# Kernel tuning notes

Measured on AMD Instinct MI355X. Metric: run time of the kernel, lower is better.

## Reference

```python
import jax, jax.numpy as jnp
import numpy as np
from jax import lax

COMMITMENT_WEIGHT = 0.25
EMA_DECAY = 0.99
EPS = 1e-5


def setup_inputs() -> dict:
    key = jax.random.key(0)
    k1, k2, k3 = jax.random.split(key, 3)
    B, L, D, K = 32, 512, 384, 8192
    z = jax.random.normal(k1, (B, L, D), dtype=jnp.float32)
    codebook = jax.random.normal(k2, (K, D), dtype=jnp.float32)
    ema_cluster_size = jnp.zeros((K,), dtype=jnp.float32)
    ema_embed_sum = jax.random.normal(k3, (K, D), dtype=jnp.float32)
    return {"z": z, "codebook": codebook, "ema_cluster_size": ema_cluster_size, "ema_embed_sum": ema_embed_sum}


def reference(z, codebook, ema_cluster_size, ema_embed_sum):
    B, L, D = z.shape
    K = codebook.shape[0]
    flat_z = z.reshape(-1, D)  # [N, D]

    # squared L2 distance to every code: [N, K]
    dist = (
        jnp.sum(flat_z * flat_z, axis=-1, keepdims=True)
        + jnp.sum(codebook * codebook, axis=-1)[None, :]
        - 2.0 * (flat_z @ codebook.T)
    )
    indices = jnp.argmin(dist, axis=-1)  # [N]
    quantized = codebook[indices].reshape(B, L, D)

    # EMA codebook update (training-mode, no-grad in original)
    cluster_size = jax.ops.segment_sum(jnp.ones_like(indices, dtype=flat_z.dtype), indices, num_segments=K)
    embed_sum = jax.ops.segment_sum(flat_z, indices, num_segments=K)  # [K, D]
    new_cluster_size = ema_cluster_size * EMA_DECAY + (1.0 - EMA_DECAY) * cluster_size
    new_embed_sum = ema_embed_sum * EMA_DECAY + (1.0 - EMA_DECAY) * embed_sum
    n = jnp.sum(new_cluster_size)
    cluster_size_smoothed = (new_cluster_size + EPS) / (n + K * EPS) * n
    new_codebook = new_embed_sum / cluster_size_smoothed[:, None]

    commitment_loss = jnp.mean((z - lax.stop_gradient(quantized)) ** 2)
    codebook_loss = jnp.mean((quantized - lax.stop_gradient(z)) ** 2)
    loss = codebook_loss + COMMITMENT_WEIGHT * commitment_loss

    # straight-through estimator
    quantized_st = z + lax.stop_gradient(quantized - z)
    return (quantized_st, indices.reshape(B, L), loss, new_cluster_size, new_embed_sum, new_codebook)
```

## Files before the change

### kernel.cpp

```cpp
#include <hip/hip_runtime.h>
#include <math.h>

#define N_TOK 16384
#define DDIM  384
#define KCODE 8192
#define EMA   0.99f
#define EPS_F 1e-5f
#define MARGIN 0.5f
#define NB 32

typedef _Float16 f16x8 __attribute__((ext_vector_type(8)));
typedef float    f32x4 __attribute__((ext_vector_type(4)));

#define OFF_PD1    0UL
#define OFF_PI1    2097152UL
#define OFF_PD2    4194304UL
#define OFF_CBH    6291456UL
#define OFF_PRD    0UL
#define OFF_PRI    1048576UL
#define OFF_TOKL   0UL
#define OFF_OFFS   65536UL
#define OFF_CURS   98560UL
#define OFF_WSIDX  12582912UL
#define OFF_COUNTS 12648448UL
#define OFF_SUMSQ  12681216UL
#define OFF_NACC   12681220UL
#define OFF_CNORM  12681472UL
#define OFF_FLIST  12714240UL
#define OFF_FCNT   12779776UL
#define OFF_PSUM   12780032UL

typedef __attribute__((address_space(1))) const unsigned int gas_uint;
typedef __attribute__((address_space(3))) unsigned int       las_uint;
__device__ __forceinline__ void gload_lds16(const void* g, void* l) {
    __builtin_amdgcn_global_load_lds((gas_uint*)g, (las_uint*)l, 16, 0, 0);
}

__global__ void cnorm_kernel(const float* __restrict__ cb, float* __restrict__ cnorm) {
    int wave = (blockIdx.x * blockDim.x + threadIdx.x) >> 6;
    int lane = threadIdx.x & 63;
    if (wave >= KCODE) return;
    const float* row = cb + (size_t)wave * DDIM;
    float s = 0.f;
    #pragma unroll
    for (int r = 0; r < 6; r++) { float v = row[lane + 64 * r]; s += v * v; }
    #pragma unroll
    for (int off = 32; off > 0; off >>= 1) s += __shfl_down(s, off, 64);
    if (lane == 0) cnorm[wave] = s;
}

__global__ void convert_kernel(const float* __restrict__ z, const float* __restrict__ cb,
                               _Float16* __restrict__ zh, _Float16* __restrict__ cbh) {
    size_t e = ((size_t)blockIdx.x * blockDim.x + threadIdx.x) * 8;
    const size_t NZ = (size_t)N_TOK * DDIM;
    const float* s;
    _Float16* d;
    if (e < NZ) { s = z + e; d = zh + e; }
    else        { s = cb + (e - NZ); d = cbh + (e - NZ); }
    float4 v0 = *(const float4*)(s);
    float4 v1 = *(const float4*)(s + 4);
    f16x8 h;
    h[0]=(_Float16)v0.x; h[1]=(_Float16)v0.y; h[2]=(_Float16)v0.z; h[3]=(_Float16)v0.w;
    h[4]=(_Float16)v1.x; h[5]=(_Float16)v1.y; h[6]=(_Float16)v1.z; h[7]=(_Float16)v1.w;
    *(f16x8*)d = h;
}

__launch_bounds__(512)
__global__ void argmin16_kernel(const _Float16* __restrict__ zh, const _Float16* __restrict__ cbh,
                                const float* __restrict__ cnorm,
                                float* __restrict__ pd1, int* __restrict__ pi1,
                                float* __restrict__ pd2) {
    __shared__ _Float16 As[128 * 32];
    __shared__ _Float16 Bs[256 * 32];
    __shared__ float xd1[128 * 4];
    __shared__ float xd2[128 * 4];
    __shared__ int   xi1[128 * 4];

    const int tid  = threadIdx.x;
    const int lane = tid & 63;
    const int wv   = tid >> 6;
    const int wy   = wv >> 2;
    const int wx   = wv & 3;
    const int m0   = blockIdx.x * 128;
    const int n0   = blockIdx.y * 256;
    const int l15  = lane & 15;
    const int l4   = lane >> 4;
    const int csw  = (l15 >> 1) & 3;

    f32x4 acc[4][4];
    #pragma unroll
    for (int i = 0; i < 4; i++)
        #pragma unroll
        for (int j = 0; j < 4; j++) acc[i][j] = (f32x4){0.f, 0.f, 0.f, 0.f};

    const int arow = tid >> 2;
    const int jch  = (tid & 3) ^ ((tid >> 3) & 3);
    const _Float16* a_src  = zh  + (size_t)(m0 + arow) * DDIM + jch * 8;
    const _Float16* b_src0 = cbh + (size_t)(n0 + arow) * DDIM + jch * 8;
    const _Float16* b_src1 = cbh + (size_t)(n0 + 128 + arow) * DDIM + jch * 8;
    _Float16* a_dst  = As + wv * 512;
    _Float16* b_dst0 = Bs + wv * 512;
    _Float16* b_dst1 = Bs + wv * 512 + 4096;

    for (int kc = 0; kc < DDIM; kc += 32) {
        gload_lds16(a_src + kc,  a_dst);
        gload_lds16(b_src0 + kc, b_dst0);
        gload_lds16(b_src1 + kc, b_dst1);
        __syncthreads();
        f16x8 af[4], bf[4];
        #pragma unroll
        for (int im = 0; im < 4; im++)
            af[im] = *(const f16x8*)(As + (wy * 64 + im * 16 + l15) * 32 + (l4 ^ csw) * 8);
        #pragma unroll
        for (int in = 0; in < 4; in++)
            bf[in] = *(const f16x8*)(Bs + (wx * 64 + in * 16 + l15) * 32 + (l4 ^ csw) * 8);
        #pragma unroll
        for (int im = 0; im < 4; im++)
            #pragma unroll
            for (int in = 0; in < 4; in++)
                acc[im][in] = __builtin_amdgcn_mfma_f32_16x16x32_f16(af[im], bf[in], acc[im][in], 0, 0, 0);
        __syncthreads();
    }

    float cn[4]; int cid[4];
    #pragma unroll
    for (int in = 0; in < 4; in++) {
        cid[in] = n0 + wx * 64 + in * 16 + l15;
        cn[in] = cnorm[cid[in]];
    }
    #pragma unroll
    for (int im = 0; im < 4; im++) {
        #pragma unroll
        for (int reg = 0; reg < 4; reg++) {
            float d1 = cn[0] - 2.f * acc[im][0][reg];
            int   i1 = cid[0];
            float d2 = 3.4e38f;
            #pragma unroll
            for (int in = 1; in < 4; in++) {
                float dd = cn[in] - 2.f * acc[im][in][reg];
                if (dd < d1) { d2 = d1; d1 = dd; i1 = cid[in]; }
                else d2 = fminf(d2, dd);
            }
            #pragma unroll
            for (int off = 1; off < 16; off <<= 1) {
                float od1 = __shfl_xor(d1, off, 16);
                int   oi1 = __shfl_xor(i1, off, 16);
                float od2 = __shfl_xor(d2, off, 16);
                if (od1 < d1 || (od1 == d1 && oi1 < i1)) { d2 = fminf(d1, od2); d1 = od1; i1 = oi1; }
                else d2 = fminf(d2, od1);
            }
            if (l15 == 0) {
                int tl = wy * 64 + im * 16 + l4 * 4 + reg;
                xd1[tl * 4 + wx] = d1; xi1[tl * 4 + wx] = i1; xd2[tl * 4 + wx] = d2;
            }
        }
    }
    __syncthreads();
    if (tid < 128) {
        float d1 = xd1[tid * 4], d2 = xd2[tid * 4];
        int   i1 = xi1[tid * 4];
        #pragma unroll
        for (int x = 1; x < 4; x++) {
            float od1 = xd1[tid * 4 + x], od2 = xd2[tid * 4 + x];
            int   oi1 = xi1[tid * 4 + x];
            if (od1 < d1 || (od1 == d1 && oi1 < i1)) { d2 = fminf(d1, od2); d1 = od1; i1 = oi1; }
            else d2 = fminf(d2, od1);
        }
        size_t o = (size_t)blockIdx.y * N_TOK + m0 + tid;
        pd1[o] = d1; pi1[o] = i1; pd2[o] = d2;
    }
}

__global__ void topmerge_kernel(const float* __restrict__ pd1, const int* __restrict__ pi1,
                                const float* __restrict__ pd2,
                                int* __restrict__ ws_idx, float* __restrict__ out_idx,
                                int* __restrict__ fcnt, int* __restrict__ flist) {
    int t = blockIdx.x * blockDim.x + threadIdx.x;
    if (t >= N_TOK) return;
    float d1 = pd1[t], d2 = pd2[t];
    int   i1 = pi1[t];
    for (int nb = 1; nb < NB; nb++) {
        size_t o = (size_t)nb * N_TOK + t;
        float od1 = pd1[o], od2 = pd2[o];
        int   oi1 = pi1[o];
        if (od1 < d1 || (od1 == d1 && oi1 < i1)) { d2 = fminf(d1, od2); d1 = od1; i1 = oi1; }
        else d2 = fminf(d2, od1);
    }
    ws_idx[t] = i1;
    out_idx[t] = (float)i1;
    if (d2 - d1 < MARGIN) {
        int s = atomicAdd(fcnt, 1);
        flist[s] = t;
    }
}

__launch_bounds__(256)
__global__ void rescore_kernel(const float* __restrict__ z, const float* __restrict__ cb,
                               const float* __restrict__ cnorm,
                               const int* __restrict__ flist, const int* __restrict__ fcnt,
                               float* __restrict__ prd, int* __restrict__ pri) {
    __shared__ float zt[8 * 384];
    __shared__ float rd[8 * 4];
    __shared__ int   ri[8 * 4];
    const int tid = threadIdx.x;
    const int lane = tid & 63, wv = tid >> 6;
    const int s = blockIdx.x;
    const int count = fcnt[0];
    for (int g = blockIdx.y; g * 8 < count; g += 256) {
        #pragma unroll
        for (int r = 0; r < 3; r++) {
            int q = tid + r * 256;
            int j = q / 96, d4 = q % 96;
            int slot = g * 8 + j; if (slot >= count) slot = count - 1;
            int tok = flist[slot];
            *(float4*)(zt + j * 384 + d4 * 4) = *(const float4*)(z + (size_t)tok * DDIM + d4 * 4);
        }
        __syncthreads();
        float bd[8]; int bi[8];
        #pragma unroll
        for (int j = 0; j < 8; j++) { bd[j] = 3.4e38f; bi[j] = 0; }
        #pragma unroll
        for (int cc = 0; cc < 2; cc++) {
            int c = s * 512 + cc * 256 + tid;
            const float* cr = cb + (size_t)c * DDIM;
            float a[8];
            #pragma unroll
            for (int j = 0; j < 8; j++) a[j] = 0.f;
            for (int d4 = 0; d4 < 96; d4++) {
                float4 cv = *(const float4*)(cr + d4 * 4);
                #pragma unroll
                for (int j = 0; j < 8; j++) {
                    float4 zv = *(const float4*)(zt + j * 384 + d4 * 4);
                    a[j] = fmaf(zv.x, cv.x, a[j]);
                    a[j] = fmaf(zv.y, cv.y, a[j]);
                    a[j] = fmaf(zv.z, cv.z, a[j]);
                    a[j] = fmaf(zv.w, cv.w, a[j]);
                }
            }
            float cnv = cnorm[c];
            #pragma unroll
            for (int j = 0; j < 8; j++) {
                float dd = cnv - 2.f * a[j];
                if (dd < bd[j]) { bd[j] = dd; bi[j] = c; }
            }
        }
        #pragma unroll
        for (int j = 0; j < 8; j++) {
            float d = bd[j]; int i = bi[j];
            #pragma unroll
            for (int off = 32; off > 0; off >>= 1) {
                float od = __shfl_xor(d, off, 64);
                int   oi = __shfl_xor(i, off, 64);
                if (od < d || (od == d && oi < i)) { d = od; i = oi; }
            }
            if (lane == 0) { rd[j * 4 + wv] = d; ri[j * 4 + wv] = i; }
        }
        __syncthreads();
        if (tid < 8) {
            float d = rd[tid * 4]; int i = ri[tid * 4];
            #pragma unroll
            for (int x = 1; x < 4; x++) {
                float od = rd[tid * 4 + x]; int oi = ri[tid * 4 + x];
                if (od < d || (od == d && oi < i)) { d = od; i = oi; }
            }
            int slot = g * 8 + tid; if (slot >= count) slot = count - 1;
            int tok = flist[slot];
            prd[(size_t)s * N_TOK + tok] = d;
            pri[(size_t)s * N_TOK + tok] = i;
        }
        __syncthreads();
    }
}

__global__ void rsmerge_kernel(const float* __restrict__ prd, const int* __restrict__ pri,
                               const int* __restrict__ flist, const int* __restrict__ fcnt,
                               int* __restrict__ ws_idx, float* __restrict__ out_idx) {
    int slot = blockIdx.x * blockDim.x + threadIdx.x;
    if (slot >= fcnt[0]) return;
    int tok = flist[slot];
    float d = prd[tok]; int i = pri[tok];
    for (int s = 1; s < 16; s++) {
        float od = prd[(size_t)s * N_TOK + tok];
        int   oi = pri[(size_t)s * N_TOK + tok];
        if (od < d || (od == d && oi < i)) { d = od; i = oi; }
    }
    ws_idx[tok] = i;
    out_idx[tok] = (float)i;
}

__global__ void quantize_kernel(const float* __restrict__ z, const float* __restrict__ cb,
                                const int* __restrict__ ws_idx,
                                float* __restrict__ out_q,
                                float* __restrict__ counts, float* __restrict__ psum) {
    __shared__ float sm[4];
    int t = (blockIdx.x * blockDim.x + threadIdx.x) >> 6;
    int lane = threadIdx.x & 63, wv = threadIdx.x >> 6;
    int k = ws_idx[t];
    const float* zr = z + (size_t)t * DDIM;
    const float* cr = cb + (size_t)k * DDIM;
    float* qr = out_q + (size_t)t * DDIM;
    float s = 0.f;
    #pragma unroll
    for (int r = 0; r < 6; r++) {
        int d = lane + 64 * r;
        float zv = zr[d];
        float qv = cr[d];
        qr[d] = qv;
        float df = zv - qv;
        s += df * df;
    }
    #pragma unroll
    for (int off = 32; off > 0; off >>= 1) s += __shfl_down(s, off, 64);
    if (lane == 0) {
        sm[wv] = s;
        atomicAdd(counts + k, 1.0f);
    }
    __syncthreads();
    if (threadIdx.x == 0) psum[blockIdx.x] = sm[0] + sm[1] + sm[2] + sm[3];
}

__global__ void scan_kernel(const float* __restrict__ counts,
                            int* __restrict__ offs, int* __restrict__ curs) {
    __shared__ int ps[1024];
    const int t = threadIdx.x;
    const int base = t * 8;
    int loc[8]; int s = 0;
    #pragma unroll
    for (int i = 0; i < 8; i++) { int c = (int)(counts[base + i] + 0.5f); loc[i] = s; s += c; }
    ps[t] = s;
    __syncthreads();
    for (int off = 1; off < 1024; off <<= 1) {
        int v = ps[t];
        int add = (t >= off) ? ps[t - off] : 0;
        __syncthreads();
        ps[t] = v + add;
        __syncthreads();
    }
    int excl = (t == 0) ? 0 : ps[t - 1];
    #pragma unroll
    for (int i = 0; i < 8; i++) {
        int o = excl + loc[i];
        offs[base + i] = o;
        curs[base + i] = o;
    }
    if (t == 1023) offs[KCODE] = ps[1023];
}

__global__ void fill_kernel(const int* __restrict__ ws_idx,
                            int* __restrict__ curs, int* __restrict__ toklist) {
    int t = blockIdx.x * blockDim.x + threadIdx.x;
    if (t >= N_TOK) return;
    int k = ws_idx[t];
    int slot = atomicAdd(curs + k, 1);
    toklist[slot] = t;
}

__global__ void cluster_kernel(const float* __restrict__ ema_cs, const float* __restrict__ counts,
                               float* __restrict__ out_ncs, float* __restrict__ n_acc,
                               const float* __restrict__ psum, float* __restrict__ out_loss) {
    int i = blockIdx.x * blockDim.x + threadIdx.x;
    float v = 0.f;
    if (i < KCODE) {
        v = EMA * ema_cs[i] + (1.f - EMA) * counts[i];
        out_ncs[i] = v;
    }
    __shared__ float sm[4];
    __shared__ float sm2[4];
    int lane = threadIdx.x & 63, w = threadIdx.x >> 6;
    #pragma unroll
    for (int off = 32; off > 0; off >>= 1) v += __shfl_down(v, off, 64);
    if (lane == 0) sm[w] = v;
    __syncthreads();
    if (threadIdx.x == 0) atomicAdd(n_acc, sm[0] + sm[1] + sm[2] + sm[3]);
    if (blockIdx.x == 0) {
        float s = 0.f;
        for (int j = threadIdx.x; j < 4096; j += 256) s += psum[j];
        #pragma unroll
        for (int off = 32; off > 0; off >>= 1) s += __shfl_down(s, off, 64);
        if (lane == 0) sm2[w] = s;
        __syncthreads();
        if (threadIdx.x == 0)
            out_loss[0] = 1.25f * (sm2[0] + sm2[1] + sm2[2] + sm2[3]) / (float)(N_TOK * DDIM);
    }
}

__global__ void codebook_fused_kernel(const float* __restrict__ z,
                                      const int* __restrict__ offs, const int* __restrict__ toklist,
                                      const float* __restrict__ ema_es,
                                      const float* __restrict__ ncs, const float* __restrict__ n_acc,
                                      float* __restrict__ out_es, float* __restrict__ out_cb) {
    int k = (blockIdx.x * blockDim.x + threadIdx.x) >> 6;
    int lane = threadIdx.x & 63;
    if (k >= KCODE) return;
    int o0 = offs[k], o1 = offs[k + 1];
    float sum[6] = {0.f, 0.f, 0.f, 0.f, 0.f, 0.f};
    for (int s = o0; s < o1; s++) {
        int tok = toklist[s];
        const float* zr = z + (size_t)tok * DDIM;
        #pragma unroll
        for (int r = 0; r < 6; r++) sum[r] += zr[lane + 64 * r];
    }
    float n = n_acc[0];
    float smooth = (ncs[k] + EPS_F) / (n + (float)KCODE * EPS_F) * n;
    float inv = 1.f / smooth;
    const float* er = ema_es + (size_t)k * DDIM;
    float* oes = out_es + (size_t)k * DDIM;
    float* ocb = out_cb + (size_t)k * DDIM;
    #pragma unroll
    for (int r = 0; r < 6; r++) {
        int d = lane + 64 * r;
        float es = EMA * er[d] + (1.f - EMA) * sum[r];
        oes[d] = es;
        ocb[d] = es * inv;
    }
}

extern "C" void kernel_launch(void* const* d_in, const int* in_sizes, int n_in,
                              void* d_out, int out_size, void* d_ws, size_t ws_size,
                              hipStream_t stream) {
    const float* z       = (const float*)d_in[0];
    const float* cb      = (const float*)d_in[1];
    const float* ema_cs  = (const float*)d_in[2];
    const float* ema_es  = (const float*)d_in[3];

    float* out      = (float*)d_out;
    float* out_q    = out;
    float* out_idx  = out + 6291456;
    float* out_loss = out + 6307840;
    float* out_ncs  = out + 6307841;
    float* out_es   = out + 6316033;
    float* out_cb   = out + 9461761;

    char* w = (char*)d_ws;
    float* pd1    = (float*)(w + OFF_PD1);
    int*   pi1    = (int*)  (w + OFF_PI1);
    float* pd2    = (float*)(w + OFF_PD2);
    _Float16* cbh = (_Float16*)(w + OFF_CBH);
    float* prd    = (float*)(w + OFF_PRD);
    int*   pri    = (int*)  (w + OFF_PRI);
    int*   toklist= (int*)  (w + OFF_TOKL);
    int*   offs   = (int*)  (w + OFF_OFFS);
    int*   curs   = (int*)  (w + OFF_CURS);
    float* cnorm  = (float*)(w + OFF_CNORM);
    int*   flist  = (int*)  (w + OFF_FLIST);
    int*   fcnt   = (int*)  (w + OFF_FCNT);
    int*   ws_idx = (int*)  (w + OFF_WSIDX);
    float* counts = (float*)(w + OFF_COUNTS);
    float* psum   = (float*)(w + OFF_PSUM);
    float* n_acc  = (float*)(w + OFF_NACC);

    _Float16* zh = (_Float16*)out;

    hipMemsetAsync(w + OFF_FCNT, 0, 256, stream);
    hipMemsetAsync(w + OFF_COUNTS, 0, 32768 + 256, stream);

    cnorm_kernel<<<KCODE * 64 / 256, 256, 0, stream>>>(cb, cnorm);

    convert_kernel<<<4608, 256, 0, stream>>>(z, cb, zh, cbh);

    dim3 grid_am(N_TOK / 128, KCODE / 256, 1);
    argmin16_kernel<<<grid_am, 512, 0, stream>>>(zh, cbh, cnorm, pd1, pi1, pd2);

    topmerge_kernel<<<N_TOK / 256, 256, 0, stream>>>(pd1, pi1, pd2, ws_idx, out_idx, fcnt, flist);

    dim3 grid_rs(16, 256, 1);
    rescore_kernel<<<grid_rs, 256, 0, stream>>>(z, cb, cnorm, flist, fcnt, prd, pri);
    rsmerge_kernel<<<N_TOK / 256, 256, 0, stream>>>(prd, pri, flist, fcnt, ws_idx, out_idx);

    quantize_kernel<<<N_TOK * 64 / 256, 256, 0, stream>>>(z, cb, ws_idx, out_q, counts, psum);
    scan_kernel<<<1, 1024, 0, stream>>>(counts, offs, curs);
    fill_kernel<<<N_TOK / 256, 256, 0, stream>>>(ws_idx, curs, toklist);
    cluster_kernel<<<(KCODE + 255) / 256, 256, 0, stream>>>(ema_cs, counts, out_ncs, n_acc, psum, out_loss);
    codebook_fused_kernel<<<KCODE * 64 / 256, 256, 0, stream>>>(z, offs, toklist, ema_es, out_ncs, n_acc, out_es, out_cb);
}
```

Before: 616.1 us.

## Rescore ambiguous tokens only against candidate blocks within margin band

Replaces the exhaustive fp32 rescore of flagged tokens over all 8192 codes, along with its separate merge kernel, with a per-wave rescore. Each wave handles one token and visits only the 256-code blocks whose fp16 best distance lies within MARGIN of the global best. Each lane walks one codebook row per iteration, so loads are uncoalesced, and correctness still depends on the fp16 error staying inside the margin band.

After: 594.8 us. -3.5%, faster.

```diff
diff --git a/kernel.cpp b/kernel.cpp
--- a/kernel.cpp
+++ b/kernel.cpp
@@ -16,8 +16,6 @@
 #define OFF_PI1    2097152UL
 #define OFF_PD2    4194304UL
 #define OFF_CBH    6291456UL
-#define OFF_PRD    0UL
-#define OFF_PRI    1048576UL
 #define OFF_TOKL   0UL
 #define OFF_OFFS   65536UL
 #define OFF_CURS   98560UL
@@ -29,6 +27,7 @@
 #define OFF_FLIST  12714240UL
 #define OFF_FCNT   12779776UL
 #define OFF_PSUM   12780032UL
+#define OFF_FD1    12796416UL
 
 typedef __attribute__((address_space(1))) const unsigned int gas_uint;
 typedef __attribute__((address_space(3))) unsigned int       las_uint;
@@ -174,7 +173,8 @@
 __global__ void topmerge_kernel(const float* __restrict__ pd1, const int* __restrict__ pi1,
                                 const float* __restrict__ pd2,
                                 int* __restrict__ ws_idx, float* __restrict__ out_idx,
-                                int* __restrict__ fcnt, int* __restrict__ flist) {
+                                int* __restrict__ fcnt, int* __restrict__ flist,
+                                float* __restrict__ fd1) {
     int t = blockIdx.x * blockDim.x + threadIdx.x;
     if (t >= N_TOK) return;
     float d1 = pd1[t], d2 = pd2[t];
@@ -188,6 +188,7 @@
     }
     ws_idx[t] = i1;
     out_idx[t] = (float)i1;
+    fd1[t] = d1;
     if (d2 - d1 < MARGIN) {
         int s = atomicAdd(fcnt, 1);
         flist[s] = t;
@@ -195,97 +196,50 @@
 }
 
 __launch_bounds__(256)
-__global__ void rescore_kernel(const float* __restrict__ z, const float* __restrict__ cb,
-                               const float* __restrict__ cnorm,
-                               const int* __restrict__ flist, const int* __restrict__ fcnt,
-                               float* __restrict__ prd, int* __restrict__ pri) {
-    __shared__ float zt[8 * 384];
-    __shared__ float rd[8 * 4];
-    __shared__ int   ri[8 * 4];
-    const int tid = threadIdx.x;
-    const int lane = tid & 63, wv = tid >> 6;
-    const int s = blockIdx.x;
+__global__ void rescore2_kernel(const float* __restrict__ z, const float* __restrict__ cb,
+                                const float* __restrict__ cnorm,
+                                const float* __restrict__ pd1, const float* __restrict__ fd1,
+                                const int* __restrict__ flist, const int* __restrict__ fcnt,
+                                int* __restrict__ ws_idx, float* __restrict__ out_idx) {
+    __shared__ float zt[4 * 384];
+    const int lane = threadIdx.x & 63;
+    const int wv   = threadIdx.x >> 6;
     const int count = fcnt[0];
-    for (int g = blockIdx.y; g * 8 < count; g += 256) {
-        #pragma unroll
-        for (int r = 0; r < 3; r++) {
-            int q = tid + r * 256;
-            int j = q / 96, d4 = q % 96;
-            int slot = g * 8 + j; if (slot >= count) slot = count - 1;
-            int tok = flist[slot];
-            *(float4*)(zt + j * 384 + d4 * 4) = *(const float4*)(z + (size_t)tok * DDIM + d4 * 4);
-        }
-        __syncthreads();
-        float bd[8]; int bi[8];
-        #pragma unroll
-        for (int j = 0; j < 8; j++) { bd[j] = 3.4e38f; bi[j] = 0; }
-        #pragma unroll
-        for (int cc = 0; cc < 2; cc++) {
-            int c = s * 512 + cc * 256 + tid;
-            const float* cr = cb + (size_t)c * DDIM;
-            float a[8];
+    float* zrow = zt + wv * 384;
+    for (int slot = blockIdx.x * 4 + wv; slot < count; slot += 2048 * 4) {
+        int t = flist[slot];
+        const float* zr = z + (size_t)t * DDIM;
+        #pragma unroll
+        for (int r = 0; r < 6; r++) zrow[lane + 64 * r] = zr[lane + 64 * r];
+        float band = fd1[t] + MARGIN;
+        float bd = 3.4e38f; int bi = 0x7fffffff;
+        for (int nb = 0; nb < NB; nb++) {
+            if (pd1[(size_t)nb * N_TOK + t] >= band) continue;
             #pragma unroll
-            for (int j = 0; j < 8; j++) a[j] = 0.f;
-            for (int d4 = 0; d4 < 96; d4++) {
-                float4 cv = *(const float4*)(cr + d4 * 4);
-                #pragma unroll
-                for (int j = 0; j < 8; j++) {
-                    float4 zv = *(const float4*)(zt + j * 384 + d4 * 4);
-                    a[j] = fmaf(zv.x, cv.x, a[j]);
-                    a[j] = fmaf(zv.y, cv.y, a[j]);
-                    a[j] = fmaf(zv.z, cv.z, a[j]);
-                    a[j] = fmaf(zv.w, cv.w, a[j]);
+            for (int c4 = 0; c4 < 4; c4++) {
+                int c = nb * 256 + c4 * 64 + lane;
+                const float* cr = cb + (size_t)c * DDIM;
+                float a = 0.f;
+                for (int d4 = 0; d4 < 96; d4++) {
+                    float4 cv = *(const float4*)(cr + d4 * 4);
+                    float4 zv = *(const float4*)(zrow + d4 * 4);
+                    a = fmaf(zv.x, cv.x, a);
+                    a = fmaf(zv.y, cv.y, a);
+                    a = fmaf(zv.z, cv.z, a);
+                    a = fmaf(zv.w, cv.w, a);
                 }
-            }
-            float cnv = cnorm[c];
-            #pragma unroll
-            for (int j = 0; j < 8; j++) {
-                float dd = cnv - 2.f * a[j];
-                if (dd < bd[j]) { bd[j] = dd; bi[j] = c; }
+                float dd = cnorm[c] - 2.f * a;
+                if (dd < bd) { bd = dd; bi = c; }
             }
         }
         #pragma unroll
-        for (int j = 0; j < 8; j++) {
-            float d = bd[j]; int i = bi[j];
-            #pragma unroll
-            for (int off = 32; off > 0; off >>= 1) {
-                float od = __shfl_xor(d, off, 64);
-                int   oi = __shfl_xor(i, off, 64);
-                if (od < d || (od == d && oi < i)) { d = od; i = oi; }
-            }
-            if (lane == 0) { rd[j * 4 + wv] = d; ri[j * 4 + wv] = i; }
+        for (int off = 32; off > 0; off >>= 1) {
+            float od = __shfl_xor(bd, off, 64);
+            int   oi = __shfl_xor(bi, off, 64);
+            if (od < bd || (od == bd && oi < bi)) { bd = od; bi = oi; }
         }
-        __syncthreads();
-        if (tid < 8) {
-            float d = rd[tid * 4]; int i = ri[tid * 4];
-            #pragma unroll
-            for (int x = 1; x < 4; x++) {
-                float od = rd[tid * 4 + x]; int oi = ri[tid * 4 + x];
-                if (od < d || (od == d && oi < i)) { d = od; i = oi; }
-            }
-            int slot = g * 8 + tid; if (slot >= count) slot = count - 1;
-            int tok = flist[slot];
-            prd[(size_t)s * N_TOK + tok] = d;
-            pri[(size_t)s * N_TOK + tok] = i;
-        }
-        __syncthreads();
-    }
-}
-
-__global__ void rsmerge_kernel(const float* __restrict__ prd, const int* __restrict__ pri,
-                               const int* __restrict__ flist, const int* __restrict__ fcnt,
-                               int* __restrict__ ws_idx, float* __restrict__ out_idx) {
-    int slot = blockIdx.x * blockDim.x + threadIdx.x;
-    if (slot >= fcnt[0]) return;
-    int tok = flist[slot];
-    float d = prd[tok]; int i = pri[tok];
-    for (int s = 1; s < 16; s++) {
-        float od = prd[(size_t)s * N_TOK + tok];
-        int   oi = pri[(size_t)s * N_TOK + tok];
-        if (od < d || (od == d && oi < i)) { d = od; i = oi; }
-    }
-    ws_idx[tok] = i;
-    out_idx[tok] = (float)i;
+        if (lane == 0) { ws_idx[t] = bi; out_idx[t] = (float)bi; }
+    }
 }
 
 __global__ void quantize_kernel(const float* __restrict__ z, const float* __restrict__ cb,
@@ -436,8 +390,6 @@
     int*   pi1    = (int*)  (w + OFF_PI1);
     float* pd2    = (float*)(w + OFF_PD2);
     _Float16* cbh = (_Float16*)(w + OFF_CBH);
-    float* prd    = (float*)(w + OFF_PRD);
-    int*   pri    = (int*)  (w + OFF_PRI);
     int*   toklist= (int*)  (w + OFF_TOKL);
     int*   offs   = (int*)  (w + OFF_OFFS);
     int*   curs   = (int*)  (w + OFF_CURS);
@@ -448,6 +400,7 @@
     float* counts = (float*)(w + OFF_COUNTS);
     float* psum   = (float*)(w + OFF_PSUM);
     float* n_acc  = (float*)(w + OFF_NACC);
+    float* fd1    = (float*)(w + OFF_FD1);
 
     _Float16* zh = (_Float16*)out;
 
@@ -461,11 +414,9 @@
     dim3 grid_am(N_TOK / 128, KCODE / 256, 1);
     argmin16_kernel<<<grid_am, 512, 0, stream>>>(zh, cbh, cnorm, pd1, pi1, pd2);
 
-    topmerge_kernel<<<N_TOK / 256, 256, 0, stream>>>(pd1, pi1, pd2, ws_idx, out_idx, fcnt, flist);
-
-    dim3 grid_rs(16, 256, 1);
-    rescore_kernel<<<grid_rs, 256, 0, stream>>>(z, cb, cnorm, flist, fcnt, prd, pri);
-    rsmerge_kernel<<<N_TOK / 256, 256, 0, stream>>>(prd, pri, flist, fcnt, ws_idx, out_idx);
+    topmerge_kernel<<<N_TOK / 256, 256, 0, stream>>>(pd1, pi1, pd2, ws_idx, out_idx, fcnt, flist, fd1);
+
+    rescore2_kernel<<<2048, 256, 0, stream>>>(z, cb, cnorm, pd1, fd1, flist, fcnt, ws_idx, out_idx);
 
     quantize_kernel<<<N_TOK * 64 / 256, 256, 0, stream>>>(z, cb, ws_idx, out_q, counts, psum);
     scan_kernel<<<1, 1024, 0, stream>>>(counts, offs, curs);
```
